# Kernel optimization log

Measured on AMD Instinct MI355X. Metric: run time of the kernel, lower is better.

## Reference

```python
import jax, jax.numpy as jnp
import numpy as np

B, C, H, W = 2, 256, 96, 192
GROUPS = 4
K = 9  # search_window_1d = (1, 9) -> 9 candidates, x-offsets -4..4, y-offset 0


def bilinear_sample(img, coords):
    """F.grid_sample(mode='bilinear', padding_mode='zeros', align_corners=True)
    with absolute pixel coordinates (torchvision optical-flow grid_sample wrapper:
    normalize by 2*x/(W-1)-1 then grid_sample align_corners=True == identity mapping).
    img: [B, C, H, W]; coords: [B, Hg, Wg, 2] as (x, y). Returns [B, C, Hg, Wg]."""
    Bi, Ci, Hi, Wi = img.shape
    x = coords[..., 0]
    y = coords[..., 1]
    x0 = jnp.floor(x)
    y0 = jnp.floor(y)
    wx1 = x - x0
    wy1 = y - y0
    wx0 = 1.0 - wx1
    wy0 = 1.0 - wy1
    flat = img.reshape(Bi, Ci, Hi * Wi)

    def gather(ix, iy):
        valid = (ix >= 0) & (ix <= Wi - 1) & (iy >= 0) & (iy <= Hi - 1)
        ixc = jnp.clip(ix, 0, Wi - 1).astype(jnp.int32)
        iyc = jnp.clip(iy, 0, Hi - 1).astype(jnp.int32)
        idx = (iyc * Wi + ixc).reshape(Bi, 1, -1)  # [B,1,Hg*Wg]
        g = jnp.take_along_axis(flat, idx, axis=2)  # [B,C,Hg*Wg]
        g = g.reshape(Bi, Ci, *ix.shape[1:])
        return g * valid[:, None].astype(img.dtype)

    out = (gather(x0, y0) * (wx0 * wy0)[:, None]
           + gather(x0 + 1, y0) * (wx1 * wy0)[:, None]
           + gather(x0, y0 + 1) * (wx0 * wy1)[:, None]
           + gather(x0 + 1, y0 + 1) * (wx1 * wy1)[:, None])
    return out


def setup_inputs() -> dict:
    key = jax.random.key(0)
    k1, k2, k3, k4 = jax.random.split(key, 4)
    return {
        "left_feature": jax.random.normal(k1, (B, C, H, W), dtype=jnp.float32),
        "right_feature": jax.random.normal(k2, (B, C, H, W), dtype=jnp.float32),
        "flow": jax.random.normal(k3, (B, 2, H, W), dtype=jnp.float32),
        "extra_offset": jax.random.normal(k4, (B, 2 * K, H, W), dtype=jnp.float32),
    }


def reference(left_feature, right_feature, flow, extra_offset):
    Bf, Cf, Hf, Wf = left_feature.shape
    gc = Cf // GROUPS
    dt = left_feature.dtype
    # 1d window offsets: meshgrid(arange(-4,5), arange(0,1), 'xy') -> (x, 0) pairs
    xs = jnp.arange(-4, 5, dtype=dt)
    win_offs = jnp.stack([xs, jnp.zeros_like(xs)], axis=-1)  # [K,2] (x,y)
    # extra_offset: [B, K, 2, H, W] -> [B, K, H, W, 2]
    extra = extra_offset.reshape(Bf, K, 2, Hf, Wf).transpose(0, 1, 3, 4, 2)
    offsets = win_offs[None, :, None, None, :] + extra  # [B,K,H,W,2]
    # base coords grid (x, y) + flow
    yy, xx = jnp.meshgrid(jnp.arange(Hf), jnp.arange(Wf), indexing="ij")
    base = jnp.stack([xx, yy], axis=-1).astype(dt)  # [H,W,2]
    coords = base[None] + flow.transpose(0, 2, 3, 1)  # [B,H,W,2]
    coords = coords[:, None] + offsets  # [B,K,H,W,2]
    coords = coords.reshape(Bf, K * Hf, Wf, 2)
    # All groups share identical window/dilation -> sample full right feature once.
    sampled = bilinear_sample(right_feature, coords)  # [B,C,K*H,W]
    sampled = sampled.reshape(Bf, GROUPS, gc, K, Hf, Wf)
    left = left_feature.reshape(Bf, GROUPS, gc, 1, Hf, Wf)
    corr = jnp.mean(left * sampled, axis=2)  # [B,G,K,H,W]
    return corr.reshape(Bf, GROUPS * K, Hf, Wf)
```

## Files before the change

### kernel.cpp

```cpp
#include <hip/hip_runtime.h>


namespace {
constexpr int kB = 2;
constexpr int kC = 256;
constexpr int kH = 96;
constexpr int kW = 192;
constexpr int kG = 4;
constexpr int kGC = kC / kG;
constexpr int kK = 9;
constexpr int kHW = kH * kW;
constexpr size_t kPlane = (size_t)kC * kHW;
constexpr int kTransBlocks = (kHW / 64) * (kC / 64) * kB;
constexpr int kCorrBlocks  = kB * kHW / 8;
}

typedef _Float16 half8_t __attribute__((ext_vector_type(8)));
typedef _Float16 half2_t __attribute__((ext_vector_type(2)));

struct TapMeta {
  int4   off;
  float4 wgt;
};

__device__ __forceinline__ float dot8(half8_t a, half8_t b, float acc) {
#if __has_builtin(__builtin_amdgcn_fdot2)
  #pragma unroll
  for (int i = 0; i < 4; ++i) {
    half2_t a2 = {a[2 * i], a[2 * i + 1]};
    half2_t b2 = {b[2 * i], b[2 * i + 1]};
    acc = __builtin_amdgcn_fdot2(a2, b2, acc, false);
  }
#else
  #pragma unroll
  for (int i = 0; i < 8; ++i) acc += (float)a[i] * (float)b[i];
#endif
  return acc;
}

__global__ __launch_bounds__(256) void prepass_kernel(
    const float* __restrict__ right, _Float16* __restrict__ right_t)
{
  __shared__ float tile[64][65];
  int tb = blockIdx.x;
  int pt = tb % (kHW / 64);
  int ct = (tb / (kHW / 64)) % 4;
  int b  = tb / ((kHW / 64) * 4);
  int p0 = pt * 64, c0 = ct * 64;
  const float* inb = right + (size_t)b * kPlane;
  _Float16*   outb = right_t + (size_t)b * kPlane;
  int t = threadIdx.x;
  int cl = t >> 2;
  int q  = t & 3;
  #pragma unroll
  for (int i = 0; i < 4; ++i) {
    int j = q + 4 * i;
    float4 v = *(const float4*)(inb + (size_t)(c0 + cl) * kHW + p0 + 4 * j);
    tile[cl][4 * j + 0] = v.x;
    tile[cl][4 * j + 1] = v.y;
    tile[cl][4 * j + 2] = v.z;
    tile[cl][4 * j + 3] = v.w;
  }
  __syncthreads();
  int pl8 = t >> 3;
  int c8  = t & 7;
  #pragma unroll
  for (int i = 0; i < 2; ++i) {
    int px = pl8 + 32 * i;
    half8_t hv;
    #pragma unroll
    for (int j = 0; j < 8; ++j)
      hv[j] = (_Float16)tile[8 * c8 + j][px];
    *(half8_t*)(outb + (size_t)(p0 + px) * kC + c0 + 8 * c8) = hv;
  }
}

__global__ __launch_bounds__(256, 3) void corr_fp16_kernel(
    const _Float16* __restrict__ right_t, const float* __restrict__ left,
    const float* __restrict__ flow, const float* __restrict__ extra,
    float* __restrict__ out)
{
  __shared__ TapMeta smeta[8 * kK];
  __shared__ _Float16 smleft[8][kC];
  __shared__ float smflow[20][8];

  int sb = (blockIdx.x & 7) * (kCorrBlocks / 8) + (blockIdx.x >> 3);
  int blockPix = sb * 8;
  int b    = blockPix / kHW;
  int pix0 = blockPix % kHW;

  int t = threadIdx.x;

  const float* Lb = left + (size_t)b * kPlane + (size_t)t * kHW + pix0;
  float4 lv0 = *(const float4*)(Lb);
  float4 lv1 = *(const float4*)(Lb + 4);

  float fval = 0.f;
  int fr = t >> 3, fpx = t & 7;
  if (t < 160) {
    const float* src = (fr < 2)
        ? flow  + ((size_t)b * 2  + fr)       * kHW + pix0 + fpx
        : extra + ((size_t)b * 18 + (fr - 2)) * kHW + pix0 + fpx;
    fval = *src;
  }

  if (t < 160) smflow[fr][fpx] = fval;
  {
    float lv[8] = {lv0.x, lv0.y, lv0.z, lv0.w, lv1.x, lv1.y, lv1.z, lv1.w};
    #pragma unroll
    for (int j = 0; j < 8; ++j)
      smleft[j][t] = (_Float16)lv[j];
  }
  __syncthreads();

  if (t < 8 * kK) {
    int px = t / kK;
    int k  = t - px * kK;
    int gpix = pix0 + px;
    int w = gpix % kW, h = gpix / kW;

    float bx = (float)w + smflow[0][px];
    float by = (float)h + smflow[1][px];
    float xx = bx + (float)(k - 4) + smflow[2 + 2 * k][px];
    float yy = by + smflow[2 + 2 * k + 1][px];
    float xf = floorf(xx), yf = floorf(yy);
    float fx = xx - xf, fy = yy - yf;
    int ix0 = (int)xf, iy0 = (int)yf;
    int ix1 = ix0 + 1, iy1 = iy0 + 1;
    bool vx0 = (ix0 >= 0) && (ix0 < kW);
    bool vx1 = (ix1 >= 0) && (ix1 < kW);
    bool vy0 = (iy0 >= 0) && (iy0 < kH);
    bool vy1 = (iy1 >= 0) && (iy1 < kH);
    int xc0 = min(max(ix0, 0), kW - 1);
    int xc1 = min(max(ix1, 0), kW - 1);
    int yc0 = min(max(iy0, 0), kH - 1);
    int yc1 = min(max(iy1, 0), kH - 1);
    float wx0 = 1.f - fx, wy0 = 1.f - fy;
    TapMeta m;
    m.off.x = (yc0 * kW + xc0) * kC;
    m.off.y = (yc0 * kW + xc1) * kC;
    m.off.z = (yc1 * kW + xc0) * kC;
    m.off.w = (yc1 * kW + xc1) * kC;
    m.wgt.x = wx0 * wy0 * ((vx0 && vy0) ? 1.f : 0.f);
    m.wgt.y = fx  * wy0 * ((vx1 && vy0) ? 1.f : 0.f);
    m.wgt.z = wx0 * fy  * ((vx0 && vy1) ? 1.f : 0.f);
    m.wgt.w = fx  * fy  * ((vx1 && vy1) ? 1.f : 0.f);
    smeta[t] = m;
  }

  int wv   = t >> 6;
  int lane = t & 63;
  int p    = lane >> 5;
  int cl   = lane & 31;
  int pix  = pix0 + wv * 2 + p;

  const _Float16* Rb = right_t + (size_t)b * kPlane + cl * 8;

  __syncthreads();

  half8_t l8 = *(const half8_t*)&smleft[wv * 2 + p][cl * 8];
  const TapMeta* mp = smeta + (wv * 2 + p) * kK;

  float rr[kK];
  half8_t tA[12], tB[12];

#define LOAD_TAPS(T, KB) do {                                      \
    int4 o0 = mp[(KB)].off, o1 = mp[(KB) + 1].off, o2 = mp[(KB) + 2].off; \
    T[0]  = *(const half8_t*)(Rb + o0.x);                          \
    T[1]  = *(const half8_t*)(Rb + o0.y);                          \
    T[2]  = *(const half8_t*)(Rb + o0.z);                          \
    T[3]  = *(const half8_t*)(Rb + o0.w);                          \
    T[4]  = *(const half8_t*)(Rb + o1.x);                          \
    T[5]  = *(const half8_t*)(Rb + o1.y);                          \
    T[6]  = *(const half8_t*)(Rb + o1.z);                          \
    T[7]  = *(const half8_t*)(Rb + o1.w);                          \
    T[8]  = *(const half8_t*)(Rb + o2.x);                          \
    T[9]  = *(const half8_t*)(Rb + o2.y);                          \
    T[10] = *(const half8_t*)(Rb + o2.z);                          \
    T[11] = *(const half8_t*)(Rb + o2.w);                          \
  } while (0)

#define COMP_TAPS(T, KB) do {                                      \
    _Pragma("unroll")                                              \
    for (int j = 0; j < 3; ++j) {                                  \
      float4 w4 = mp[(KB) + j].wgt;                                \
      float d00 = dot8(T[4 * j + 0], l8, 0.f);                     \
      float d01 = dot8(T[4 * j + 1], l8, 0.f);                     \
      float d10 = dot8(T[4 * j + 2], l8, 0.f);                     \
      float d11 = dot8(T[4 * j + 3], l8, 0.f);                     \
      float r = w4.x * d00 + w4.y * d01 + w4.z * d10 + w4.w * d11; \
      r += __shfl_xor(r, 1);                                       \
      r += __shfl_xor(r, 2);                                       \
      r += __shfl_xor(r, 4);                                       \
      rr[(KB) + j] = r;                                            \
    }                                                              \
  } while (0)

  LOAD_TAPS(tA, 0);
  LOAD_TAPS(tB, 3);
  __builtin_amdgcn_sched_barrier(0);
  COMP_TAPS(tA, 0);
  LOAD_TAPS(tA, 6);
  __builtin_amdgcn_sched_barrier(0);
  COMP_TAPS(tB, 3);
  COMP_TAPS(tA, 6);

#undef LOAD_TAPS
#undef COMP_TAPS

  int g = cl >> 3;
  if ((cl & 7) == 0) {
    float* outp = out + ((size_t)b * kG + g) * kK * kHW + pix;
    #pragma unroll
    for (int k = 0; k < kK; ++k)
      outp[(size_t)k * kHW] = rr[k] * (1.f / kGC);
  }
}

__global__ __launch_bounds__(256) void crestereo_corr_fallback(
    const float* __restrict__ left, const float* __restrict__ right,
    const float* __restrict__ flow, const float* __restrict__ extra,
    float* __restrict__ out)
{
  int t = blockIdx.x * blockDim.x + threadIdx.x;
  int w = t % kW;
  int h = (t / kW) % kH;
  int k = (t / kHW) % kK;
  int g = (t / (kHW * kK)) % kG;
  int b = t / (kHW * kK * kG);

  int pix = h * kW + w;
  const float* flowb = flow + b * 2 * kHW + pix;
  float x = (float)(w + (k - 4)) + flowb[0];
  float y = (float)h + flowb[kHW];
  const float* extb = extra + (size_t)(b * 2 * kK + 2 * k) * kHW + pix;
  x += extb[0];
  y += extb[kHW];

  float xf = floorf(x), yf = floorf(y);
  float fx = x - xf, fy = y - yf;
  int ix0 = (int)xf, iy0 = (int)yf;
  int ix1 = ix0 + 1, iy1 = iy0 + 1;
  bool vx0 = (ix0 >= 0) && (ix0 < kW);
  bool vx1 = (ix1 >= 0) && (ix1 < kW);
  bool vy0 = (iy0 >= 0) && (iy0 < kH);
  bool vy1 = (iy1 >= 0) && (iy1 < kH);
  int xc0 = min(max(ix0, 0), kW - 1);
  int xc1 = min(max(ix1, 0), kW - 1);
  int yc0 = min(max(iy0, 0), kH - 1);
  int yc1 = min(max(iy1, 0), kH - 1);
  float wx0 = 1.f - fx, wy0 = 1.f - fy;
  float w00 = wx0 * wy0 * ((vx0 && vy0) ? 1.f : 0.f);
  float w01 = fx  * wy0 * ((vx1 && vy0) ? 1.f : 0.f);
  float w10 = wx0 * fy  * ((vx0 && vy1) ? 1.f : 0.f);
  float w11 = fx  * fy  * ((vx1 && vy1) ? 1.f : 0.f);
  int idx = yc0 * kW + xc0;
  int dx  = xc1 - xc0;
  int dyw = (yc1 - yc0) * kW;

  const float* Rb = right + (size_t)(b * kC + g * kGC) * kHW + idx;
  const float* Lb = left  + (size_t)(b * kC + g * kGC) * kHW + pix;

  float acc = 0.f;
  #pragma unroll 4
  for (int c = 0; c < kGC; ++c) {
    const float* Rc = Rb + (size_t)c * kHW;
    float l   = Lb[(size_t)c * kHW];
    acc += l * (w00 * Rc[0] + w01 * Rc[dx] + w10 * Rc[dyw] + w11 * Rc[dx + dyw]);
  }
  out[(size_t)((b * kG + g) * kK + k) * kHW + pix] = acc * (1.f / kGC);
}

extern "C" void kernel_launch(void* const* d_in, const int* in_sizes, int n_in,
                              void* d_out, int out_size, void* d_ws, size_t ws_size,
                              hipStream_t stream) {
  const float* left  = (const float*)d_in[0];
  const float* right = (const float*)d_in[1];
  const float* flow  = (const float*)d_in[2];
  const float* extra = (const float*)d_in[3];
  float* out = (float*)d_out;

  size_t t_bytes = (size_t)kB * kPlane * sizeof(_Float16);
  if (ws_size >= t_bytes) {
    _Float16* right_t = (_Float16*)d_ws;

    prepass_kernel<<<kTransBlocks, 256, 0, stream>>>(right, right_t);
    corr_fp16_kernel<<<kCorrBlocks, 256, 0, stream>>>(
        right_t, left, flow, extra, out);
  } else {
    int total = kB * kG * kK * kH * kW;
    crestereo_corr_fallback<<<(total + 255) / 256, 256, 0, stream>>>(
        left, right, flow, extra, out);
  }
}
```

Measured before the change: 136.9 us.

## Process 16 pixels per 512-thread block and stage output through shared memory

```diff
diff --git a/kernel.cpp b/kernel.cpp
--- a/kernel.cpp
+++ b/kernel.cpp
@@ -12,7 +12,8 @@
 constexpr int kHW = kH * kW;
 constexpr size_t kPlane = (size_t)kC * kHW;
 constexpr int kTransBlocks = (kHW / 64) * (kC / 64) * kB;
-constexpr int kCorrBlocks  = kB * kHW / 8;
+constexpr int kPx = 16;
+constexpr int kCorrBlocks  = kB * kHW / kPx;
 }
 
 typedef _Float16 half8_t __attribute__((ext_vector_type(8)));
@@ -75,45 +76,45 @@
   }
 }
 
-__global__ __launch_bounds__(256, 3) void corr_fp16_kernel(
+__global__ __launch_bounds__(512, 4) void corr_fp16_kernel(
     const _Float16* __restrict__ right_t, const float* __restrict__ left,
     const float* __restrict__ flow, const float* __restrict__ extra,
     float* __restrict__ out)
 {
-  __shared__ TapMeta smeta[8 * kK];
-  __shared__ _Float16 smleft[8][kC];
-  __shared__ float smflow[20][8];
+  __shared__ _Float16 smleft[kPx][kC];
+  __shared__ float    smflow[20][kPx];
+  __shared__ TapMeta  smeta[kPx * kK];
+  __shared__ float    smout[kG * kK][kPx];
 
   int sb = (blockIdx.x & 7) * (kCorrBlocks / 8) + (blockIdx.x >> 3);
-  int blockPix = sb * 8;
+  int blockPix = sb * kPx;
   int b    = blockPix / kHW;
   int pix0 = blockPix % kHW;
 
   int t = threadIdx.x;
 
-  const float* Lb = left + (size_t)b * kPlane + (size_t)t * kHW + pix0;
-  float4 lv0 = *(const float4*)(Lb);
-  float4 lv1 = *(const float4*)(Lb + 4);
-
-  float fval = 0.f;
-  int fr = t >> 3, fpx = t & 7;
-  if (t < 160) {
+  #pragma unroll
+  for (int it = 0; it < 2; ++it) {
+    int c = (t >> 2) + 128 * it;
+    int q = t & 3;
+    float4 v = *(const float4*)(left + (size_t)b * kPlane +
+                                (size_t)c * kHW + pix0 + 4 * q);
+    smleft[4 * q + 0][c] = (_Float16)v.x;
+    smleft[4 * q + 1][c] = (_Float16)v.y;
+    smleft[4 * q + 2][c] = (_Float16)v.z;
+    smleft[4 * q + 3][c] = (_Float16)v.w;
+  }
+
+  if (t < 320) {
+    int fr = t >> 4, fpx = t & 15;
     const float* src = (fr < 2)
         ? flow  + ((size_t)b * 2  + fr)       * kHW + pix0 + fpx
         : extra + ((size_t)b * 18 + (fr - 2)) * kHW + pix0 + fpx;
-    fval = *src;
-  }
-
-  if (t < 160) smflow[fr][fpx] = fval;
-  {
-    float lv[8] = {lv0.x, lv0.y, lv0.z, lv0.w, lv1.x, lv1.y, lv1.z, lv1.w};
-    #pragma unroll
-    for (int j = 0; j < 8; ++j)
-      smleft[j][t] = (_Float16)lv[j];
+    smflow[fr][fpx] = *src;
   }
   __syncthreads();
 
-  if (t < 8 * kK) {
+  if (t < kPx * kK) {
     int px = t / kK;
     int k  = t - px * kK;
     int gpix = pix0 + px;
@@ -152,14 +153,14 @@
   int lane = t & 63;
   int p    = lane >> 5;
   int cl   = lane & 31;
-  int pix  = pix0 + wv * 2 + p;
+  int px   = wv * 2 + p;
 
   const _Float16* Rb = right_t + (size_t)b * kPlane + cl * 8;
 
   __syncthreads();
 
-  half8_t l8 = *(const half8_t*)&smleft[wv * 2 + p][cl * 8];
-  const TapMeta* mp = smeta + (wv * 2 + p) * kK;
+  half8_t l8 = *(const half8_t*)&smleft[px][cl * 8];
+  const TapMeta* mp = smeta + px * kK;
 
   float rr[kK];
   half8_t tA[12], tB[12];
@@ -208,12 +209,22 @@
 #undef LOAD_TAPS
 #undef COMP_TAPS
 
-  int g = cl >> 3;
   if ((cl & 7) == 0) {
-    float* outp = out + ((size_t)b * kG + g) * kK * kHW + pix;
+    int g = cl >> 3;
     #pragma unroll
     for (int k = 0; k < kK; ++k)
-      outp[(size_t)k * kHW] = rr[k] * (1.f / kGC);
+      smout[g * kK + k][px] = rr[k] * (1.f / kGC);
+  }
+  __syncthreads();
+  {
+    float* ob = out + (size_t)b * kG * kK * kHW + pix0;
+    int r   = t >> 4;
+    int px2 = t & 15;
+    ob[(size_t)r * kHW + px2] = smout[r][px2];
+    if (t < (kG * kK - 32) * kPx) {
+      int r2 = 32 + (t >> 4);
+      ob[(size_t)r2 * kHW + px2] = smout[r2][px2];
+    }
   }
 }
 
@@ -285,7 +296,7 @@
     _Float16* right_t = (_Float16*)d_ws;
 
     prepass_kernel<<<kTransBlocks, 256, 0, stream>>>(right, right_t);
-    corr_fp16_kernel<<<kCorrBlocks, 256, 0, stream>>>(
+    corr_fp16_kernel<<<kCorrBlocks, 512, 0, stream>>>(
         right_t, left, flow, extra, out);
   } else {
     int total = kB * kG * kK * kH * kW;
```

After: 136.9 us. Within noise of the previous version (-0.0%).
